# Kernel optimization log

Hardware: AMD Instinct MI355X
Metric: run time of the kernel (lower is better)

## Reference

```python
import jax, jax.numpy as jnp
import numpy as np

C = 64
HW = 21 * 21  # 441
NEIGHBOR_K = 3


def setup_inputs() -> dict:
    key = jax.random.key(0)
    k1, k2, k3, k4 = jax.random.split(key, 4)
    B1, B2 = 32, 25
    x1 = jax.random.normal(k1, (B1, C, 21, 21), dtype=jnp.float32)
    x2 = jax.random.normal(k2, (B2, C, 21, 21), dtype=jnp.float32)
    mask1 = jax.random.uniform(k3, (B1, 21, 21), dtype=jnp.float32)
    mask2 = jax.random.uniform(k4, (B2, 21, 21), dtype=jnp.float32)
    return {"x1": x1, "x2": x2, "mask1": mask1, "mask2": mask2}


def reference(x1, x2, mask1, mask2):
    B1 = x1.shape[0]
    B2 = x2.shape[0]
    q = x1.reshape(B1, C, HW)  # (B1, 64, 441) query descriptors
    s = x2.reshape(B2, C, HW)  # (B2, 64, 441) support descriptors
    # per-descriptor L2 norms over channel dim
    qn = jnp.linalg.norm(q, axis=1)  # (B1, 441)
    sn = jnp.linalg.norm(s, axis=1)  # (B2, 441)
    # cosine similarity between every query descriptor and every support descriptor
    inner = jnp.einsum('aci,bcj->abij', q, s)  # (B1, B2, 441, 441)
    sim = inner / (qn[:, None, :, None] * sn[None, :, None, :])
    # mask out invalid spatial positions on both sides
    sim = sim * mask1.reshape(B1, 1, HW, 1) * mask2.reshape(1, B2, 1, HW)
    # top-k nearest support descriptors per query descriptor, sum over all
    topk_vals, _ = jax.lax.top_k(sim, NEIGHBOR_K)  # (B1, B2, 441, k)
    return topk_vals.reshape(B1, B2, -1).sum(axis=2)  # (B1, B2)
```

## Files before the change

### kernel.cpp

```cpp
#include <hip/hip_runtime.h>
#include <math.h>

#define CCH 64
#define HW 441
#define HWP 448
#define NT 28
#define NB2 25
#define PANEL (HWP * CCH)

typedef _Float16 half8 __attribute__((ext_vector_type(8)));
typedef __fp16 h2 __attribute__((ext_vector_type(2)));
typedef float f32x4 __attribute__((ext_vector_type(4)));

__global__ void normalize_frag_kernel(const float* __restrict__ x1,
                                      const float* __restrict__ m1,
                                      const float* __restrict__ x2,
                                      const float* __restrict__ m2,
                                      _Float16* __restrict__ qh,
                                      _Float16* __restrict__ sh,
                                      float* __restrict__ out, int nout,
                                      int n1rows, int nrows) {
    int idx = blockIdx.x * blockDim.x + threadIdx.x;
    if (idx < nout) out[idx] = 0.f;
    if (idx >= nrows) return;
    const float* x; const float* mk; _Float16* outp; int rb;
    if (idx < n1rows) { x = x1; mk = m1; outp = qh; rb = idx; }
    else             { x = x2; mk = m2; outp = sh; rb = idx - n1rows; }
    int b = rb / HWP, i = rb - b * HWP;
    float vals[CCH];
    if (i < HW) {
        const float* xb = x + (size_t)b * CCH * HW + i;
        float ss = 0.f;
#pragma unroll
        for (int c = 0; c < CCH; ++c) { float v = xb[c * HW]; vals[c] = v; ss += v * v; }
        float scale = mk[b * HW + i] * rsqrtf(ss);
#pragma unroll
        for (int c = 0; c < CCH; ++c) vals[c] *= scale;
    } else {
#pragma unroll
        for (int c = 0; c < CCH; ++c) vals[c] = 0.f;
    }
    _Float16* pb = outp + (size_t)b * PANEL + (i >> 4) * 1024 + (i & 15) * 8;
#pragma unroll
    for (int f = 0; f < 2; ++f) {
#pragma unroll
        for (int qd = 0; qd < 4; ++qd) {
            half8 h;
#pragma unroll
            for (int e = 0; e < 8; ++e) h[e] = (_Float16)vals[f * 32 + qd * 8 + e];
            *(half8*)(pb + f * 512 + qd * 128) = h;
        }
    }
}

static __device__ __forceinline__ h2 hmax2(h2 a, h2 b) {
    return __builtin_elementwise_max(a, b);
}
static __device__ __forceinline__ h2 hmin2(h2 a, h2 b) {
    return __builtin_elementwise_min(a, b);
}

#define PK_INSERT(v, p0, p1, p2)           \
    do {                                   \
        h2 _m = hmax2(p0, v);              \
        h2 _c = hmin2(p0, v);              \
        p0 = _m;                           \
        _m = hmax2(p1, _c);                \
        _c = hmin2(p1, _c);                \
        p1 = _m;                           \
        p2 = hmax2(p2, _c);                \
    } while (0)

#define MERGE3(t0, t1, t2, b0, b1, b2)            \
    do {                                          \
        float _m0 = fmaxf(t0, b0);                \
        float _n0 = fminf(t0, b0);                \
        float _m1 = fmaxf(t1, b1);                \
        float _t2 = fmaxf(t2, b2);                \
        t0 = _m0;                                 \
        t1 = fmaxf(_n0, _m1);                     \
        t2 = fmaxf(fminf(_n0, _m1), _t2);         \
    } while (0)

template <int NI>
__device__ __forceinline__ float do_pass(const _Float16* __restrict__ qtiles,
                                         const _Float16* __restrict__ spanel,
                                         int lane, int quad) {
    const float NEG = -1e30f;
    const f32x4 FZ = {0.f, 0.f, 0.f, 0.f};
    const h2 NEGH = {(__fp16)-65504.f, (__fp16)-65504.f};
    half8 bf0[NI], bf1[NI];
#pragma unroll
    for (int t = 0; t < NI; ++t) {
        const _Float16* qp = qtiles + t * 1024 + lane * 8;
        bf0[t] = *(const half8*)qp;
        bf1[t] = *(const half8*)(qp + 512);
    }
    h2 p0[NI], p1[NI], p2[NI];
#pragma unroll
    for (int t = 0; t < NI; ++t) { p0[t] = NEGH; p1[t] = NEGH; p2[t] = NEGH; }

    const _Float16* sp = spanel + lane * 8;
    half8 a0 = *(const half8*)sp;
    half8 a1 = *(const half8*)(sp + 512);

    for (int jt = 0; jt < NT - 1; ++jt) {
        const _Float16* np = sp + (jt + 1) * 1024;
        half8 na0 = *(const half8*)np;
        half8 na1 = *(const half8*)(np + 512);
#pragma unroll
        for (int t = 0; t < NI; ++t) {
            f32x4 z = __builtin_amdgcn_mfma_f32_16x16x32_f16(a0, bf0[t], FZ, 0, 0, 0);
            z = __builtin_amdgcn_mfma_f32_16x16x32_f16(a1, bf1[t], z, 0, 0, 0);
            h2 c02 = __builtin_amdgcn_cvt_pkrtz(z[0], z[2]);
            h2 c13 = __builtin_amdgcn_cvt_pkrtz(z[1], z[3]);
            PK_INSERT(c02, p0[t], p1[t], p2[t]);
            PK_INSERT(c13, p0[t], p1[t], p2[t]);
        }
        a0 = na0;
        a1 = na1;
    }
    {
#pragma unroll
        for (int t = 0; t < NI; ++t) {
            f32x4 z = __builtin_amdgcn_mfma_f32_16x16x32_f16(a0, bf0[t], FZ, 0, 0, 0);
            z = __builtin_amdgcn_mfma_f32_16x16x32_f16(a1, bf1[t], z, 0, 0, 0);
#pragma unroll
            for (int r = 0; r < 4; ++r)
                if (quad * 4 + r >= 9) z[r] = NEG;
            h2 c02 = __builtin_amdgcn_cvt_pkrtz(z[0], z[2]);
            h2 c13 = __builtin_amdgcn_cvt_pkrtz(z[1], z[3]);
            PK_INSERT(c02, p0[t], p1[t], p2[t]);
            PK_INSERT(c13, p0[t], p1[t], p2[t]);
        }
    }

    float res = 0.f;
#pragma unroll
    for (int t = 0; t < NI; ++t) {
        float t0 = (float)p0[t][0], t1 = (float)p1[t][0], t2 = (float)p2[t][0];
        float b0 = (float)p0[t][1], b1 = (float)p1[t][1], b2 = (float)p2[t][1];
        MERGE3(t0, t1, t2, b0, b1, b2);
        b0 = __shfl_xor(t0, 16); b1 = __shfl_xor(t1, 16); b2 = __shfl_xor(t2, 16);
        MERGE3(t0, t1, t2, b0, b1, b2);
        b0 = __shfl_xor(t0, 32); b1 = __shfl_xor(t1, 32); b2 = __shfl_xor(t2, 32);
        MERGE3(t0, t1, t2, b0, b1, b2);
        res += t0 + t1 + t2;
    }
    return (quad == 0) ? res : 0.f;
}

__global__ __launch_bounds__(128, 4) void sim_topk_mfma(const _Float16* __restrict__ qh,
                                                        const _Float16* __restrict__ sh,
                                                        float* __restrict__ out) {
    int blk = blockIdx.x;
    int pair = blk >> 2, g = blk & 3;
    int a = pair / NB2, b = pair - a * NB2;
    int tid = threadIdx.x, wave = tid >> 6, lane = tid & 63, quad = lane >> 4;
    const _Float16* qtiles = qh + (size_t)a * PANEL + (size_t)g * 7 * 1024;
    const _Float16* spanel = sh + (size_t)b * PANEL;

    float wacc = (wave == 0)
                     ? do_pass<4>(qtiles, spanel, lane, quad)
                     : do_pass<3>(qtiles + 4 * 1024, spanel, lane, quad);

#pragma unroll
    for (int off = 32; off > 0; off >>= 1) wacc += __shfl_down(wacc, off);
    if (lane == 0) atomicAdd(&out[pair], wacc);
}

extern "C" void kernel_launch(void* const* d_in, const int* in_sizes, int n_in,
                              void* d_out, int out_size, void* d_ws, size_t ws_size,
                              hipStream_t stream) {
    const float* x1 = (const float*)d_in[0];
    const float* x2 = (const float*)d_in[1];
    const float* m1 = (const float*)d_in[2];
    const float* m2 = (const float*)d_in[3];
    float* out = (float*)d_out;

    int B1 = in_sizes[0] / (CCH * HW);
    int B2 = in_sizes[1] / (CCH * HW);

    _Float16* qh = (_Float16*)d_ws;
    _Float16* sh = qh + (size_t)B1 * PANEL;

    int n1 = B1 * HWP, ntot = (B1 + B2) * HWP;
    normalize_frag_kernel<<<(ntot + 255) / 256, 256, 0, stream>>>(
        x1, m1, x2, m2, qh, sh, out, B1 * B2, n1, ntot);
    sim_topk_mfma<<<B1 * B2 * 4, 128, 0, stream>>>(qh, sh, out);
}
```

Before: 101.5 us.

## Give each wave seven query tiles, prefetch support two tiles ahead, shrink normalize blocks

Each wave now handles 7 query tiles against the full support panel instead of 3-4, which halves the number of blocks and doubles the reuse of each support fragment load across MFMAs. Support loads are prefetched two tiles ahead rather than one, to hide more global-memory latency. The normalize kernel switches to 64-thread blocks to spread its rows across more CUs. The trade-off is higher register pressure from 7 sets of B fragments and top-3 state under launch_bounds(128,4), which could cause spills or lower occupancy.

Measured after the change: 99.94 us. About the same (-1.6%).

```diff
diff --git a/kernel.cpp b/kernel.cpp
--- a/kernel.cpp
+++ b/kernel.cpp
@@ -12,14 +12,11 @@
 typedef __fp16 h2 __attribute__((ext_vector_type(2)));
 typedef float f32x4 __attribute__((ext_vector_type(4)));
 
-__global__ void normalize_frag_kernel(const float* __restrict__ x1,
-                                      const float* __restrict__ m1,
-                                      const float* __restrict__ x2,
-                                      const float* __restrict__ m2,
-                                      _Float16* __restrict__ qh,
-                                      _Float16* __restrict__ sh,
-                                      float* __restrict__ out, int nout,
-                                      int n1rows, int nrows) {
+__global__ __launch_bounds__(64) void normalize_frag_kernel(
+        const float* __restrict__ x1, const float* __restrict__ m1,
+        const float* __restrict__ x2, const float* __restrict__ m2,
+        _Float16* __restrict__ qh, _Float16* __restrict__ sh,
+        float* __restrict__ out, int nout, int n1rows, int nrows) {
     int idx = blockIdx.x * blockDim.x + threadIdx.x;
     if (idx < nout) out[idx] = 0.f;
     if (idx >= nrows) return;
@@ -101,30 +98,32 @@
     for (int t = 0; t < NI; ++t) { p0[t] = NEGH; p1[t] = NEGH; p2[t] = NEGH; }
 
     const _Float16* sp = spanel + lane * 8;
-    half8 a0 = *(const half8*)sp;
-    half8 a1 = *(const half8*)(sp + 512);
+    half8 c0 = *(const half8*)sp;
+    half8 c1 = *(const half8*)(sp + 512);
+    half8 n0 = *(const half8*)(sp + 1024);
+    half8 n1 = *(const half8*)(sp + 1024 + 512);
 
     for (int jt = 0; jt < NT - 1; ++jt) {
-        const _Float16* np = sp + (jt + 1) * 1024;
-        half8 na0 = *(const half8*)np;
-        half8 na1 = *(const half8*)(np + 512);
+        int pf = (jt + 2 < NT) ? jt + 2 : NT - 1;
+        const _Float16* pp = sp + pf * 1024;
+        half8 f0 = *(const half8*)pp;
+        half8 f1 = *(const half8*)(pp + 512);
 #pragma unroll
         for (int t = 0; t < NI; ++t) {
-            f32x4 z = __builtin_amdgcn_mfma_f32_16x16x32_f16(a0, bf0[t], FZ, 0, 0, 0);
-            z = __builtin_amdgcn_mfma_f32_16x16x32_f16(a1, bf1[t], z, 0, 0, 0);
+            f32x4 z = __builtin_amdgcn_mfma_f32_16x16x32_f16(c0, bf0[t], FZ, 0, 0, 0);
+            z = __builtin_amdgcn_mfma_f32_16x16x32_f16(c1, bf1[t], z, 0, 0, 0);
             h2 c02 = __builtin_amdgcn_cvt_pkrtz(z[0], z[2]);
             h2 c13 = __builtin_amdgcn_cvt_pkrtz(z[1], z[3]);
             PK_INSERT(c02, p0[t], p1[t], p2[t]);
             PK_INSERT(c13, p0[t], p1[t], p2[t]);
         }
-        a0 = na0;
-        a1 = na1;
+        c0 = n0; c1 = n1; n0 = f0; n1 = f1;
     }
     {
 #pragma unroll
         for (int t = 0; t < NI; ++t) {
-            f32x4 z = __builtin_amdgcn_mfma_f32_16x16x32_f16(a0, bf0[t], FZ, 0, 0, 0);
-            z = __builtin_amdgcn_mfma_f32_16x16x32_f16(a1, bf1[t], z, 0, 0, 0);
+            f32x4 z = __builtin_amdgcn_mfma_f32_16x16x32_f16(c0, bf0[t], FZ, 0, 0, 0);
+            z = __builtin_amdgcn_mfma_f32_16x16x32_f16(c1, bf1[t], z, 0, 0, 0);
 #pragma unroll
             for (int r = 0; r < 4; ++r)
                 if (quad * 4 + r >= 9) z[r] = NEG;
@@ -154,15 +153,14 @@
                                                         const _Float16* __restrict__ sh,
                                                         float* __restrict__ out) {
     int blk = blockIdx.x;
-    int pair = blk >> 2, g = blk & 3;
+    int pair = blk >> 1, g = blk & 1;
     int a = pair / NB2, b = pair - a * NB2;
     int tid = threadIdx.x, wave = tid >> 6, lane = tid & 63, quad = lane >> 4;
-    const _Float16* qtiles = qh + (size_t)a * PANEL + (size_t)g * 7 * 1024;
+    int group = g * 2 + wave;
+    const _Float16* qtiles = qh + (size_t)a * PANEL + (size_t)group * 7 * 1024;
     const _Float16* spanel = sh + (size_t)b * PANEL;
 
-    float wacc = (wave == 0)
-                     ? do_pass<4>(qtiles, spanel, lane, quad)
-                     : do_pass<3>(qtiles + 4 * 1024, spanel, lane, quad);
+    float wacc = do_pass<7>(qtiles, spanel, lane, quad);
 
 #pragma unroll
     for (int off = 32; off > 0; off >>= 1) wacc += __shfl_down(wacc, off);
@@ -185,7 +183,7 @@
     _Float16* sh = qh + (size_t)B1 * PANEL;
 
     int n1 = B1 * HWP, ntot = (B1 + B2) * HWP;
-    normalize_frag_kernel<<<(ntot + 255) / 256, 256, 0, stream>>>(
+    normalize_frag_kernel<<<(ntot + 63) / 64, 64, 0, stream>>>(
         x1, m1, x2, m2, qh, sh, out, B1 * B2, n1, ntot);
-    sim_topk_mfma<<<B1 * B2 * 4, 128, 0, stream>>>(qh, sh, out);
+    sim_topk_mfma<<<B1 * B2 * 2, 128, 0, stream>>>(qh, sh, out);
 }
```
